# Optimization experiments

Measured on AMD Instinct MI355X. Metric: run time of the kernel, lower is better.

Reference implementation:

```python
import jax, jax.numpy as jnp
import numpy as np

DIM = 512

def setup_inputs() -> dict:
    key = jax.random.key(0)
    kx, kq, kk, kv = jax.random.split(key, 4)
    x = jax.random.normal(kx, (8, 2048, DIM), dtype=jnp.float32)
    # Dense kernels are [in_dim, out_dim], no bias
    Wq = jax.random.normal(kq, (DIM, DIM), dtype=jnp.float32) * (DIM ** -0.5)
    Wk = jax.random.normal(kk, (DIM, DIM), dtype=jnp.float32) * (DIM ** -0.5)
    Wv = jax.random.normal(kv, (DIM, DIM), dtype=jnp.float32) * (DIM ** -0.5)
    return {"x": x, "Wq": Wq, "Wk": Wk, "Wv": Wv}

def reference(x, Wq, Wk, Wv):
    # x: [b, s, d]
    q = jnp.einsum('bsd,de->bse', x, Wq)
    k = jnp.einsum('bsd,de->bse', x, Wk)
    v = jnp.einsum('bsd,de->bse', x, Wv)
    scale = jnp.sqrt(jnp.asarray(DIM, dtype=x.dtype))
    attn = jnp.einsum('bqe,bke->bqk', q, k) / scale  # [b, s, s]
    attn = jax.nn.softmax(attn, axis=-1)
    return jnp.einsum('bqk,bke->bqe', attn, v)  # [b, s, d]
```

## Files before the change

kernel.cpp:

```cpp
#include <hip/hip_runtime.h>
#include <stdint.h>

typedef unsigned short u16;
typedef unsigned int u32;
typedef float floatx4 __attribute__((ext_vector_type(4)));
typedef __bf16 bf16x8 __attribute__((ext_vector_type(8)));
typedef __attribute__((address_space(1))) const u32 gu32;
typedef __attribute__((address_space(3))) u32 lu32;

#define SEQ 2048
#define DIM 512
#define NBATCH 8

__device__ __forceinline__ u16 f2bf(float f) {
  u32 u = __float_as_uint(f);
  u += 0x7fffu + ((u >> 16) & 1u);
  return (u16)(u >> 16);
}

__device__ __forceinline__ void stage_tile64(const u16* __restrict__ g, int ld, int k0, u16* lds) {
  const int t = threadIdx.x;
  const int wave = t >> 6, lane = t & 63;
  const int rsub = lane >> 3;
  const int lg = (lane & 7) ^ rsub;
#pragma unroll
  for (int q = 0; q < 4; ++q) {
    const int chunk = wave * 4 + q;
    const int row = chunk * 8 + rsub;
    const u16* gp = g + (size_t)row * ld + k0 + lg * 8;
    u16* lp = lds + chunk * 512 + lane * 8;
    __builtin_amdgcn_global_load_lds((gu32*)gp, (lu32*)lp, 16, 0, 0);
  }
}

__device__ __forceinline__ void gemm_core(const u16* A, const u16* BT, int lda, int ldb, int kdim,
                                          u16* As, u16* Bs, floatx4 acc[4][4]) {
  const int t = threadIdx.x;
  const int wave = t >> 6, lane = t & 63;
  const int wr = (wave >> 1) * 64, wc = (wave & 1) * 64;
  const int l15 = lane & 15, quad = lane >> 4;
  const int swz = l15 & 7;
  for (int k0 = 0; k0 < kdim; k0 += 64) {
    stage_tile64(A, lda, k0, As);
    stage_tile64(BT, ldb, k0, Bs);
    __syncthreads();
#pragma unroll
    for (int ks = 0; ks < 2; ++ks) {
      const int pg = ((ks << 2) + quad) ^ swz;
      bf16x8 af[4], bfr[4];
#pragma unroll
      for (int i = 0; i < 4; ++i) {
        af[i]  = *(const bf16x8*)(As + (wr + i * 16 + l15) * 64 + pg * 8);
        bfr[i] = *(const bf16x8*)(Bs + (wc + i * 16 + l15) * 64 + pg * 8);
      }
#pragma unroll
      for (int mi = 0; mi < 4; ++mi)
#pragma unroll
        for (int ni = 0; ni < 4; ++ni)
          acc[mi][ni] = __builtin_amdgcn_mfma_f32_16x16x32_bf16(af[mi], bfr[ni], acc[mi][ni], 0, 0, 0);
    }
    __syncthreads();
  }
}

__device__ __forceinline__ void zero_acc(floatx4 acc[4][4]) {
#pragma unroll
  for (int i = 0; i < 4; ++i)
#pragma unroll
    for (int j = 0; j < 4; ++j)
      acc[i][j] = (floatx4){0.f, 0.f, 0.f, 0.f};
}

__global__ __launch_bounds__(256) void k_cvt_x(const float* __restrict__ x, u16* __restrict__ xb) {
  size_t i = ((size_t)blockIdx.x * 256 + threadIdx.x) * 8;
  float4 a = *(const float4*)(x + i);
  float4 b = *(const float4*)(x + i + 4);
  u16 o[8] = {f2bf(a.x), f2bf(a.y), f2bf(a.z), f2bf(a.w),
              f2bf(b.x), f2bf(b.y), f2bf(b.z), f2bf(b.w)};
  *(uint4*)(xb + i) = *(const uint4*)o;
}

__global__ __launch_bounds__(256) void k_pack_w(const float* __restrict__ Wq, const float* __restrict__ Wk,
                                                const float* __restrict__ Wv, u16* __restrict__ wt) {
  int t = blockIdx.x * 256 + threadIdx.x;
  int k = t & 511, n = t >> 9;
  int sec = n >> 9, nc = n & 511;
  const float* W = (sec == 0) ? Wq : (sec == 1) ? Wk : Wv;
  wt[(size_t)n * 512 + k] = f2bf(W[(size_t)k * 512 + nc]);
}

__global__ __launch_bounds__(256) void k_qkv(const u16* __restrict__ xb, const u16* __restrict__ wt,
                                             u16* __restrict__ qo, u16* __restrict__ ko,
                                             u16* __restrict__ vt) {
  __shared__ __align__(16) u16 As[128 * 64];
  __shared__ __align__(16) u16 Bs[128 * 64];
  const int m0 = blockIdx.x * 128, n0 = blockIdx.y * 128;
  floatx4 acc[4][4];
  zero_acc(acc);
  gemm_core(xb + (size_t)m0 * DIM, wt + (size_t)n0 * DIM, DIM, DIM, DIM, As, Bs, acc);
  const int t = threadIdx.x, wave = t >> 6, lane = t & 63;
  const int wr = (wave >> 1) * 64, wc = (wave & 1) * 64;
  const int l15 = lane & 15, quad = lane >> 4;
  const int sec = n0 >> 9;
#pragma unroll
  for (int mi = 0; mi < 4; ++mi)
#pragma unroll
    for (int ni = 0; ni < 4; ++ni)
#pragma unroll
      for (int r = 0; r < 4; ++r) {
        int m = m0 + wr + mi * 16 + quad * 4 + r;
        int n = n0 + wc + ni * 16 + l15;
        float v = acc[mi][ni][r];
        int nc = n & 511;
        if (sec == 0) {
          qo[(size_t)m * DIM + nc] = f2bf(v * 0.04419417382415922f);
        } else if (sec == 1) {
          ko[(size_t)m * DIM + nc] = f2bf(v);
        } else {
          int b = m >> 11, s = m & 2047;
          vt[((size_t)(b * DIM + nc)) * SEQ + s] = f2bf(v);
        }
      }
}

__global__ __launch_bounds__(256) void k_scores(const u16* __restrict__ q, const u16* __restrict__ kk,
                                                u16* __restrict__ sc, float* __restrict__ rowsum,
                                                int b0) {
  __shared__ __align__(16) u16 As[128 * 64];
  __shared__ __align__(16) u16 Bs[128 * 64];
  const int bz = blockIdx.z, bb = b0 + bz;
  const int m0 = blockIdx.x * 128, n0 = blockIdx.y * 128;
  floatx4 acc[4][4];
  zero_acc(acc);
  gemm_core(q + (size_t)bb * SEQ * DIM + (size_t)m0 * DIM,
            kk + (size_t)bb * SEQ * DIM + (size_t)n0 * DIM, DIM, DIM, DIM, As, Bs, acc);
  u16* C = sc + (size_t)bz * SEQ * SEQ;
  float* rsb = rowsum + (size_t)bb * SEQ;
  const int t = threadIdx.x, wave = t >> 6, lane = t & 63;
  const int wr = (wave >> 1) * 64, wc = (wave & 1) * 64;
  const int l15 = lane & 15, quad = lane >> 4;
#pragma unroll
  for (int mi = 0; mi < 4; ++mi)
#pragma unroll
    for (int r = 0; r < 4; ++r) {
      int m = m0 + wr + mi * 16 + quad * 4 + r;
      float p = 0.f;
#pragma unroll
      for (int ni = 0; ni < 4; ++ni) {
        int n = n0 + wc + ni * 16 + l15;
        float e = __expf(acc[mi][ni][r]);
        C[(size_t)m * SEQ + n] = f2bf(e);
        p += e;
      }
      p += __shfl_xor(p, 1); p += __shfl_xor(p, 2);
      p += __shfl_xor(p, 4); p += __shfl_xor(p, 8);
      if (l15 == 0) atomicAdd(&rsb[m], p);
    }
}

__global__ __launch_bounds__(256) void k_pv(const u16* __restrict__ sc, const u16* __restrict__ vt,
                                            const float* __restrict__ rowsum,
                                            float* __restrict__ out, int b0) {
  __shared__ __align__(16) u16 As[128 * 64];
  __shared__ __align__(16) u16 Bs[128 * 64];
  const int bz = blockIdx.z, bb = b0 + bz;
  const int m0 = blockIdx.x * 128, n0 = blockIdx.y * 128;
  floatx4 acc[4][4];
  zero_acc(acc);
  gemm_core(sc + (size_t)bz * SEQ * SEQ + (size_t)m0 * SEQ,
            vt + (size_t)bb * DIM * SEQ + (size_t)n0 * SEQ, SEQ, SEQ, SEQ, As, Bs, acc);
  float* C = out + (size_t)bb * SEQ * DIM;
  const float* rsb = rowsum + (size_t)bb * SEQ;
  const int t = threadIdx.x, wave = t >> 6, lane = t & 63;
  const int wr = (wave >> 1) * 64, wc = (wave & 1) * 64;
  const int l15 = lane & 15, quad = lane >> 4;
#pragma unroll
  for (int mi = 0; mi < 4; ++mi)
#pragma unroll
    for (int r = 0; r < 4; ++r) {
      int m = m0 + wr + mi * 16 + quad * 4 + r;
      float inv = 1.0f / rsb[m];
#pragma unroll
      for (int ni = 0; ni < 4; ++ni) {
        int n = n0 + wc + ni * 16 + l15;
        C[(size_t)m * DIM + n] = acc[mi][ni][r] * inv;
      }
    }
}

extern "C" void kernel_launch(void* const* d_in, const int* in_sizes, int n_in,
                              void* d_out, int out_size, void* d_ws, size_t ws_size,
                              hipStream_t stream) {
  const float* x  = (const float*)d_in[0];
  const float* Wq = (const float*)d_in[1];
  const float* Wk = (const float*)d_in[2];
  const float* Wv = (const float*)d_in[3];
  float* out = (float*)d_out;
  char* ws = (char*)d_ws;

  u16* xb   = (u16*)(ws + 0);
  u16* wt   = (u16*)(ws + 16777216);
  u16* qo   = (u16*)(ws + 18350080);
  u16* ko   = (u16*)(ws + 35127296);
  u16* vt   = (u16*)(ws + 51904512);
  float* rs = (float*)(ws + 68681728);
  u16* sc   = (u16*)(ws + 68747264);
  const size_t base_need = 68747264;
  const size_t per_b = (size_t)SEQ * SEQ * 2;
  size_t avail = (ws_size > base_need) ? (ws_size - base_need) : 0;
  int nb = (int)(avail / per_b);
  if (nb < 1) nb = 1;
  if (nb > NBATCH) nb = NBATCH;

  hipMemsetAsync(rs, 0, (size_t)NBATCH * SEQ * sizeof(float), stream);
  k_cvt_x<<<dim3(4096), dim3(256), 0, stream>>>(x, xb);
  k_pack_w<<<dim3(3072), dim3(256), 0, stream>>>(Wq, Wk, Wv, wt);
  k_qkv<<<dim3(128, 12), dim3(256), 0, stream>>>(xb, wt, qo, ko, vt);
  for (int b0 = 0; b0 < NBATCH; b0 += nb) {
    int nbr = (NBATCH - b0 < nb) ? (NBATCH - b0) : nb;
    k_scores<<<dim3(16, 16, nbr), dim3(256), 0, stream>>>(qo, ko, sc, rs, b0);
    k_pv<<<dim3(16, 4, nbr), dim3(256), 0, stream>>>(sc, vt, rs, out, b0);
  }
}
```

Measured before the change: 248.7 us.

## Fuse prep kernels, tile weight transpose, remap blocks for XCD locality, add occupancy hints

Merges x conversion and weight packing into one launch and rewrites the weight transpose to go through an LDS tile, so both reads and writes are coalesced. Block indices in the scores and PV kernels are remapped so that blocks sharing operand rows land on the same XCD, which should raise L2 reuse. Also adds launch_bounds occupancy hints, uses the hardware packed bf16 convert when the builtin exists, and computes the exponentials before the stores. The XCD remap assumes blocks are dispatched round-robin across eight XCDs.

```diff
diff --git a/kernel.cpp b/kernel.cpp
--- a/kernel.cpp
+++ b/kernel.cpp
@@ -12,10 +12,25 @@
 #define DIM 512
 #define NBATCH 8
 
+#if defined(__has_builtin)
+#if __has_builtin(__builtin_amdgcn_cvt_pk_bf16_f32)
+#define HAVE_PK_BF16 1
+#endif
+#endif
+#ifndef HAVE_PK_BF16
+#define HAVE_PK_BF16 0
+#endif
+
 __device__ __forceinline__ u16 f2bf(float f) {
+#if HAVE_PK_BF16
+  auto p = __builtin_amdgcn_cvt_pk_bf16_f32(f, f);
+  union { decltype(p) v; u16 u[2]; } cv; cv.v = p;
+  return cv.u[0];
+#else
   u32 u = __float_as_uint(f);
   u += 0x7fffu + ((u >> 16) & 1u);
   return (u16)(u >> 16);
+#endif
 }
 
 __device__ __forceinline__ void stage_tile64(const u16* __restrict__ g, int ld, int k0, u16* lds) {
@@ -71,27 +86,43 @@
       acc[i][j] = (floatx4){0.f, 0.f, 0.f, 0.f};
 }
 
-__global__ __launch_bounds__(256) void k_cvt_x(const float* __restrict__ x, u16* __restrict__ xb) {
-  size_t i = ((size_t)blockIdx.x * 256 + threadIdx.x) * 8;
-  float4 a = *(const float4*)(x + i);
-  float4 b = *(const float4*)(x + i + 4);
-  u16 o[8] = {f2bf(a.x), f2bf(a.y), f2bf(a.z), f2bf(a.w),
-              f2bf(b.x), f2bf(b.y), f2bf(b.z), f2bf(b.w)};
-  *(uint4*)(xb + i) = *(const uint4*)o;
-}
-
-__global__ __launch_bounds__(256) void k_pack_w(const float* __restrict__ Wq, const float* __restrict__ Wk,
-                                                const float* __restrict__ Wv, u16* __restrict__ wt) {
-  int t = blockIdx.x * 256 + threadIdx.x;
-  int k = t & 511, n = t >> 9;
-  int sec = n >> 9, nc = n & 511;
+__global__ __launch_bounds__(256) void k_prep(const float* __restrict__ x,
+                                              const float* __restrict__ Wq, const float* __restrict__ Wk,
+                                              const float* __restrict__ Wv,
+                                              u16* __restrict__ xb, u16* __restrict__ wt) {
+  __shared__ float tile[64][65];
+  const int t = threadIdx.x;
+  if (blockIdx.x < 4096) {
+    size_t i = ((size_t)blockIdx.x * 256 + t) * 8;
+    float4 a = *(const float4*)(x + i);
+    float4 b = *(const float4*)(x + i + 4);
+    u16 o[8] = {f2bf(a.x), f2bf(a.y), f2bf(a.z), f2bf(a.w),
+                f2bf(b.x), f2bf(b.y), f2bf(b.z), f2bf(b.w)};
+    *(uint4*)(xb + i) = *(const uint4*)o;
+    return;
+  }
+  const int r = blockIdx.x - 4096;
+  const int sec = r >> 6, rem = r & 63;
+  const int kb = (rem & 7) * 64, nb0 = (rem >> 3) * 64;
   const float* W = (sec == 0) ? Wq : (sec == 1) ? Wk : Wv;
-  wt[(size_t)n * 512 + k] = f2bf(W[(size_t)k * 512 + nc]);
-}
-
-__global__ __launch_bounds__(256) void k_qkv(const u16* __restrict__ xb, const u16* __restrict__ wt,
-                                             u16* __restrict__ qo, u16* __restrict__ ko,
-                                             u16* __restrict__ vt) {
+#pragma unroll
+  for (int i = 0; i < 4; ++i) {
+    int kr = i * 16 + (t >> 4), nc = (t & 15) * 4;
+    float4 v = *(const float4*)&W[(size_t)(kb + kr) * 512 + nb0 + nc];
+    tile[kr][nc] = v.x; tile[kr][nc + 1] = v.y; tile[kr][nc + 2] = v.z; tile[kr][nc + 3] = v.w;
+  }
+  __syncthreads();
+#pragma unroll
+  for (int i = 0; i < 4; ++i) {
+    int nr = i * 16 + (t >> 4), kc = (t & 15) * 4;
+    u16 o[4] = {f2bf(tile[kc][nr]), f2bf(tile[kc + 1][nr]), f2bf(tile[kc + 2][nr]), f2bf(tile[kc + 3][nr])};
+    *(uint2*)&wt[(size_t)(sec * 512 + nb0 + nr) * 512 + kb + kc] = *(const uint2*)o;
+  }
+}
+
+__global__ __launch_bounds__(256, 4) void k_qkv(const u16* __restrict__ xb, const u16* __restrict__ wt,
+                                                u16* __restrict__ qo, u16* __restrict__ ko,
+                                                u16* __restrict__ vt) {
   __shared__ __align__(16) u16 As[128 * 64];
   __shared__ __align__(16) u16 Bs[128 * 64];
   const int m0 = blockIdx.x * 128, n0 = blockIdx.y * 128;
@@ -123,13 +154,14 @@
       }
 }
 
-__global__ __launch_bounds__(256) void k_scores(const u16* __restrict__ q, const u16* __restrict__ kk,
-                                                u16* __restrict__ sc, float* __restrict__ rowsum,
-                                                int b0) {
+__global__ __launch_bounds__(256, 4) void k_scores(const u16* __restrict__ q, const u16* __restrict__ kk,
+                                                   u16* __restrict__ sc, float* __restrict__ rowsum,
+                                                   int b0) {
   __shared__ __align__(16) u16 As[128 * 64];
   __shared__ __align__(16) u16 Bs[128 * 64];
   const int bz = blockIdx.z, bb = b0 + bz;
-  const int m0 = blockIdx.x * 128, n0 = blockIdx.y * 128;
+  const int xcd = blockIdx.x & 7, j = blockIdx.x >> 3;
+  const int m0 = (j & 15) * 128, n0 = (xcd * 2 + (j >> 4)) * 128;
   floatx4 acc[4][4];
   zero_acc(acc);
   gemm_core(q + (size_t)bb * SEQ * DIM + (size_t)m0 * DIM,
@@ -145,12 +177,16 @@
     for (int r = 0; r < 4; ++r) {
       int m = m0 + wr + mi * 16 + quad * 4 + r;
       float p = 0.f;
+      float ev[4];
+#pragma unroll
+      for (int ni = 0; ni < 4; ++ni) {
+        ev[ni] = __expf(acc[mi][ni][r]);
+        p += ev[ni];
+      }
 #pragma unroll
       for (int ni = 0; ni < 4; ++ni) {
         int n = n0 + wc + ni * 16 + l15;
-        float e = __expf(acc[mi][ni][r]);
-        C[(size_t)m * SEQ + n] = f2bf(e);
-        p += e;
+        C[(size_t)m * SEQ + n] = f2bf(ev[ni]);
       }
       p += __shfl_xor(p, 1); p += __shfl_xor(p, 2);
       p += __shfl_xor(p, 4); p += __shfl_xor(p, 8);
@@ -158,13 +194,14 @@
     }
 }
 
-__global__ __launch_bounds__(256) void k_pv(const u16* __restrict__ sc, const u16* __restrict__ vt,
-                                            const float* __restrict__ rowsum,
-                                            float* __restrict__ out, int b0) {
+__global__ __launch_bounds__(256, 4) void k_pv(const u16* __restrict__ sc, const u16* __restrict__ vt,
+                                               const float* __restrict__ rowsum,
+                                               float* __restrict__ out, int b0) {
   __shared__ __align__(16) u16 As[128 * 64];
   __shared__ __align__(16) u16 Bs[128 * 64];
   const int bz = blockIdx.z, bb = b0 + bz;
-  const int m0 = blockIdx.x * 128, n0 = blockIdx.y * 128;
+  const int xcd = blockIdx.x & 7, j = blockIdx.x >> 3;
+  const int m0 = (xcd * 2 + (j & 1)) * 128, n0 = (j >> 1) * 128;
   floatx4 acc[4][4];
   zero_acc(acc);
   gemm_core(sc + (size_t)bz * SEQ * SEQ + (size_t)m0 * SEQ,
@@ -213,12 +250,11 @@
   if (nb > NBATCH) nb = NBATCH;
 
   hipMemsetAsync(rs, 0, (size_t)NBATCH * SEQ * sizeof(float), stream);
-  k_cvt_x<<<dim3(4096), dim3(256), 0, stream>>>(x, xb);
-  k_pack_w<<<dim3(3072), dim3(256), 0, stream>>>(Wq, Wk, Wv, wt);
+  k_prep<<<dim3(4288), dim3(256), 0, stream>>>(x, Wq, Wk, Wv, xb, wt);
   k_qkv<<<dim3(128, 12), dim3(256), 0, stream>>>(xb, wt, qo, ko, vt);
   for (int b0 = 0; b0 < NBATCH; b0 += nb) {
     int nbr = (NBATCH - b0 < nb) ? (NBATCH - b0) : nb;
-    k_scores<<<dim3(16, 16, nbr), dim3(256), 0, stream>>>(qo, ko, sc, rs, b0);
-    k_pv<<<dim3(16, 4, nbr), dim3(256), 0, stream>>>(sc, vt, rs, out, b0);
-  }
-}
+    k_scores<<<dim3(256, 1, nbr), dim3(256), 0, stream>>>(qo, ko, sc, rs, b0);
+    k_pv<<<dim3(64, 1, nbr), dim3(256), 0, stream>>>(sc, vt, rs, out, b0);
+  }
+}
```

Measured after the change: 216.0 us. 1.15x faster.
